# Kernel tuning notes

Measured on AMD Instinct MI355X. Metric: run time of the kernel, lower is better.

Reference implementation:

```python
import jax, jax.numpy as jnp
import numpy as np

D = 1024          # dim_in == dim_out
H = 16            # num_heads
G = 4             # num_kv_groups
HD = D // H       # head_dim = 64
GS = H // G       # group_size = 4
S = 2048          # context_length / seq_len
B = 2
EPS = 1e-05


def setup_inputs() -> dict:
    key = jax.random.key(0)
    ks = jax.random.split(key, 12)
    sd = 0.02
    return {
        "x":  jax.random.normal(ks[0], (B, S, D), jnp.float32),
        # torch.nn.Linear weights are stored [out_features, in_features]
        "wq": jax.random.normal(ks[1], (D, D), jnp.float32) * sd,
        "wk": jax.random.normal(ks[2], (G * HD, D), jnp.float32) * sd,
        "wv": jax.random.normal(ks[3], (G * HD, D), jnp.float32) * sd,
        "wo": jax.random.normal(ks[4], (D, D), jnp.float32) * sd,
        "w1": jax.random.normal(ks[5], (4 * D, D), jnp.float32) * sd,
        "w2": jax.random.normal(ks[6], (D, 4 * D), jnp.float32) * sd,
        "g1": jnp.ones((D,), jnp.float32),
        "b1": jnp.zeros((D,), jnp.float32),
        "g2": jnp.ones((D,), jnp.float32),
        "b2": jnp.zeros((D,), jnp.float32),
    }


def _layernorm(x, gamma, beta):
    mean = jnp.mean(x, axis=-1, keepdims=True)
    var = jnp.var(x, axis=-1, keepdims=True)  # unbiased=False
    return (x - mean) * jax.lax.rsqrt(var + EPS) * gamma + beta


def _gelu_tanh(x):
    c = jnp.sqrt(jnp.asarray(2.0 / jnp.pi, x.dtype))
    return 0.5 * x * (1.0 + jnp.tanh(c * (x + 0.044715 * x ** 3)))


def _gqa(x, wq, wk, wv, wo):
    b, s, _ = x.shape
    q = (x @ wq.T).reshape(b, s, H, HD).transpose(0, 2, 1, 3)   # [B,H,S,hd]
    k = (x @ wk.T).reshape(b, s, G, HD).transpose(0, 2, 1, 3)   # [B,G,S,hd]
    v = (x @ wv.T).reshape(b, s, G, HD).transpose(0, 2, 1, 3)
    k = jnp.repeat(k, GS, axis=1)                               # [B,H,S,hd]
    v = jnp.repeat(v, GS, axis=1)
    scores = jnp.einsum('bhqd,bhkd->bhqk', q, k)                # [B,H,S,S]
    causal = jnp.tril(jnp.ones((s, s), bool))
    scores = jnp.where(causal, scores, -jnp.inf)
    attn = jax.nn.softmax(scores / jnp.sqrt(jnp.asarray(HD, scores.dtype)), axis=-1)
    ctx = jnp.einsum('bhqk,bhkd->bhqd', attn, v)                # [B,H,S,hd]
    ctx = ctx.transpose(0, 2, 1, 3).reshape(b, s, D)
    return ctx @ wo.T


def reference(x, wq, wk, wv, wo, w1, w2, g1, b1, g2, b2):
    h = x + _gqa(_layernorm(x, g1, b1), wq, wk, wv, wo)
    ff = _layernorm(h, g2, b2) @ w1.T
    ff = _gelu_tanh(ff) @ w2.T
    return h + ff
```

## Files before the change

kernel.cpp:

```cpp
#include <hip/hip_runtime.h>
#include <stdint.h>

typedef __bf16 bf16_t;
typedef bf16_t bf16x8 __attribute__((ext_vector_type(8)));
typedef bf16_t bf16x4 __attribute__((ext_vector_type(4)));
typedef float f32x4 __attribute__((ext_vector_type(4)));

#define DEVFN static __device__ __forceinline__

DEVFN void gload_lds16(const void* g, void* l) {
  __builtin_amdgcn_global_load_lds((const __attribute__((address_space(1))) void*)g,
                                   (__attribute__((address_space(3))) void*)l, 16, 0, 0);
}

DEVFN float gelu_f(float x) {
  float u = 0.7978845608028654f * (x + 0.044715f * x * x * x);
  float e = __expf(2.0f * u);
  float t = 1.0f - 2.0f / (e + 1.0f);
  return 0.5f * x * (1.0f + t);
}

template <int CTRL>
DEVFN float dpp_rot(float x) {
  int i = __builtin_bit_cast(int, x);
  int r = __builtin_amdgcn_update_dpp(i, i, CTRL, 0xF, 0xF, false);
  return __builtin_bit_cast(float, r);
}
DEVFN float dpp_sum16(float x) {
  x += dpp_rot<0x121>(x);
  x += dpp_rot<0x122>(x);
  x += dpp_rot<0x124>(x);
  x += dpp_rot<0x128>(x);
  return x;
}

DEVFN void ln_row_body(const float* __restrict__ in, const float* __restrict__ gamma,
                       const float* __restrict__ beta, bf16_t* __restrict__ out,
                       int row, int tid, float* ss, float* qs) {
  const float4 v = ((const float4*)(in + (size_t)row * 1024))[tid];
  float s = v.x + v.y + v.z + v.w;
  float q = v.x * v.x + v.y * v.y + v.z * v.z + v.w * v.w;
#pragma unroll
  for (int off = 1; off < 64; off <<= 1) {
    s += __shfl_xor(s, off);
    q += __shfl_xor(q, off);
  }
  if ((tid & 63) == 0) { ss[tid >> 6] = s; qs[tid >> 6] = q; }
  __syncthreads();
  s = ss[0] + ss[1] + ss[2] + ss[3];
  q = qs[0] + qs[1] + qs[2] + qs[3];
  const float mean = s * (1.0f / 1024.0f);
  const float var = q * (1.0f / 1024.0f) - mean * mean;
  const float rstd = rsqrtf(var + 1e-5f);
  const float4 g4 = ((const float4*)gamma)[tid];
  const float4 b4 = ((const float4*)beta)[tid];
  bf16x4 o;
  o[0] = (bf16_t)((v.x - mean) * rstd * g4.x + b4.x);
  o[1] = (bf16_t)((v.y - mean) * rstd * g4.y + b4.y);
  o[2] = (bf16_t)((v.z - mean) * rstd * g4.z + b4.z);
  o[3] = (bf16_t)((v.w - mean) * rstd * g4.w + b4.w);
  *(bf16x4*)(out + (size_t)row * 1024 + tid * 4) = o;
}

DEVFN void cvt_quad(const float* __restrict__ s, bf16_t* __restrict__ d, int j) {
  float4 v = ((const float4*)s)[j];
  bf16x4 o;
  o[0] = (bf16_t)v.x; o[1] = (bf16_t)v.y; o[2] = (bf16_t)v.z; o[3] = (bf16_t)v.w;
  ((bf16x4*)d)[j] = o;
}

static __device__ const int kPrefix16[16] = {0,1,2,3,4,6,8,10,12,15,18,21,24,28,32,36};

DEVFN void combine_body(const bf16_t* __restrict__ pO, const float* __restrict__ pL,
                        bf16_t* __restrict__ ctx, int i, int h, int b, int tid) {
  const int C = (i >> 2) + 1;
  const int base = (b * 16 + h) * 40 + kPrefix16[i];
  const int row = tid >> 1;
  const int half = (tid & 1) * 32;
  float L = 0.0f, acc[32];
#pragma unroll
  for (int e = 0; e < 32; ++e) acc[e] = 0.0f;
  for (int c = 0; c < C; ++c) {
    L += pL[(size_t)(base + c) * 128 + row];
    const bf16_t* op = pO + ((size_t)(base + c) * 128 + row) * 64 + half;
#pragma unroll
    for (int j = 0; j < 4; ++j) {
      bf16x8 v = *(const bf16x8*)(op + j * 8);
#pragma unroll
      for (int e = 0; e < 8; ++e) acc[j * 8 + e] += (float)v[e];
    }
  }
  const float inv = 1.0f / L;
  bf16_t* outp = ctx + ((size_t)b * 2048 + i * 128 + row) * 1024 + h * 64 + half;
#pragma unroll
  for (int j = 0; j < 4; ++j) {
    bf16x8 o;
#pragma unroll
    for (int e = 0; e < 8; ++e) o[e] = (bf16_t)(acc[j * 8 + e] * inv);
    *(bf16x8*)(outp + j * 8) = o;
  }
}

__global__ __launch_bounds__(256) void prep1_kernel(const float* __restrict__ x,
                                                    const float* __restrict__ g1,
                                                    const float* __restrict__ b1,
                                                    bf16_t* __restrict__ h1,
                                                    const float* __restrict__ wq,
                                                    const float* __restrict__ wk,
                                                    const float* __restrict__ wv,
                                                    const float* __restrict__ wo,
                                                    bf16_t* __restrict__ qkv_dst,
                                                    bf16_t* __restrict__ wo_dst) {
  __shared__ float ss[4], qs[4];
  if (blockIdx.x < 4096) {
    ln_row_body(x, g1, b1, h1, blockIdx.x, threadIdx.x, ss, qs);
  } else {
    int i = (blockIdx.x - 4096) * 256 + threadIdx.x;
    const int stride = 2048 * 256;
    for (; i < 655360; i += stride) {
      if (i < 262144)      cvt_quad(wq, qkv_dst, i);
      else if (i < 327680) cvt_quad(wk, qkv_dst + 1048576, i - 262144);
      else if (i < 393216) cvt_quad(wv, qkv_dst + 1310720, i - 327680);
      else                 cvt_quad(wo, wo_dst, i - 393216);
    }
  }
}

__global__ __launch_bounds__(256) void prep2_kernel(const bf16_t* __restrict__ pO,
                                                    const float* __restrict__ pL,
                                                    bf16_t* __restrict__ ctx,
                                                    const float* __restrict__ w1,
                                                    bf16_t* __restrict__ w1_b) {
  if (blockIdx.x < 512) {
    const int i = blockIdx.x & 15;
    const int h = (blockIdx.x >> 4) & 15;
    const int b = blockIdx.x >> 8;
    combine_body(pO, pL, ctx, i, h, b, threadIdx.x);
  } else {
    const int i = (blockIdx.x - 512) * 256 + threadIdx.x;
    cvt_quad(w1, w1_b, i);
  }
}

__global__ __launch_bounds__(256) void prep3_kernel(const float* __restrict__ hres,
                                                    const float* __restrict__ g2,
                                                    const float* __restrict__ b2,
                                                    bf16_t* __restrict__ h2,
                                                    const float* __restrict__ w2,
                                                    bf16_t* __restrict__ w2_b) {
  __shared__ float ss[4], qs[4];
  if (blockIdx.x < 4096) {
    ln_row_body(hres, g2, b2, h2, blockIdx.x, threadIdx.x, ss, qs);
  } else {
    const int i = (blockIdx.x - 4096) * 256 + threadIdx.x;
    cvt_quad(w2, w2_b, i);
  }
}

template <int EPI, int BM>
__global__ __launch_bounds__(256, (BM == 64 ? 3 : 2))
void gemm_bt(const bf16_t* __restrict__ A, const bf16_t* __restrict__ W,
             bf16_t* outb, float* outf, const float* resid, int M, int N, int K) {
  constexpr int MI = BM / 32;
  constexpr int WRS = BM / 2;
  __shared__ __align__(16) bf16_t As[2][2][BM * 32];
  __shared__ __align__(16) bf16_t Bs[2][2][128 * 32];
  const int tid = threadIdx.x;
  const int lane = tid & 63;
  const int wid = tid >> 6;
  const int l15 = lane & 15;
  const int l4 = lane >> 4;

  const int nwg = gridDim.x * gridDim.y;
  const int bid = blockIdx.y * gridDim.x + blockIdx.x;
  const int cpx = nwg >> 3;
  const int swz = (bid & 7) * cpx + (bid >> 3);
  const int m0 = (swz / gridDim.x) * BM;
  const int n0 = (swz % gridDim.x) * 128;

  const int wr = wid >> 1;
  const int wc = wid & 1;

  const int sr = lane >> 2;
  const int sk = (lane & 3) * 8;
  const bf16_t* aBase;
  if constexpr (BM == 128) aBase = A + (size_t)(m0 + wid * 32 + sr) * K + sk;
  else                     aBase = A + (size_t)(m0 + wid * 16 + sr) * K + sk;
  const bf16_t* bBase = W + (size_t)(n0 + wid * 32 + sr) * K + sk;
  const size_t rowOff16 = (size_t)16 * K;

  f32x4 acc[MI][4] = {};
  const int NT = K / 64;

  auto stage = [&](int buf, int t) {
    const int kt = t * 64;
#pragma unroll
    for (int kk = 0; kk < 2; ++kk) {
      const int ko = kt + kk * 32;
      if constexpr (BM == 128) {
        gload_lds16(aBase + ko, &As[buf][kk][wid * 1024]);
        gload_lds16(aBase + ko + rowOff16, &As[buf][kk][wid * 1024 + 512]);
      } else {
        gload_lds16(aBase + ko, &As[buf][kk][wid * 512]);
      }
      gload_lds16(bBase + ko, &Bs[buf][kk][wid * 1024]);
      gload_lds16(bBase + ko + rowOff16, &Bs[buf][kk][wid * 1024 + 512]);
    }
  };

  stage(0, 0);
  for (int t = 0; t < NT; ++t) {
    __syncthreads();
    if (t + 1 < NT) stage((t + 1) & 1, t + 1);
    const int buf = t & 1;
#pragma unroll
    for (int kk = 0; kk < 2; ++kk) {
      bf16x8 af[MI], bfr[4];
#pragma unroll
      for (int i = 0; i < MI; ++i)
        af[i] = *(const bf16x8*)&As[buf][kk][(wr * WRS + i * 16 + l15) * 32 + l4 * 8];
#pragma unroll
      for (int j = 0; j < 4; ++j)
        bfr[j] = *(const bf16x8*)&Bs[buf][kk][(wc * 64 + j * 16 + l15) * 32 + l4 * 8];
#pragma unroll
      for (int i = 0; i < MI; ++i)
#pragma unroll
        for (int j = 0; j < 4; ++j)
          acc[i][j] = __builtin_amdgcn_mfma_f32_16x16x32_bf16(af[i], bfr[j], acc[i][j], 0, 0, 0);
    }
  }

  const int col0 = n0 + wc * 64 + l15;
  const int row0 = m0 + wr * WRS + l4 * 4;
#pragma unroll
  for (int i = 0; i < MI; ++i) {
#pragma unroll
    for (int r = 0; r < 4; ++r) {
      const size_t row = (size_t)(row0 + i * 16 + r);
#pragma unroll
      for (int j = 0; j < 4; ++j) {
        const size_t idx = row * N + col0 + j * 16;
        const float v = acc[i][j][r];
        if constexpr (EPI == 0) {
          outb[idx] = (bf16_t)v;
        } else if constexpr (EPI == 1) {
          outb[idx] = (bf16_t)gelu_f(v);
        } else {
          outf[idx] = resid[idx] + v;
        }
      }
    }
  }
}

static __device__ const int kQbTab[40] = {0,1,2,3,4,4,5,5,6,6,7,7,8,8,8,9,9,9,10,10,10,
                                          11,11,11,12,12,12,12,13,13,13,13,14,14,14,14,15,15,15,15};
static __device__ const int kCTab[40]  = {0,0,0,0,0,1,0,1,0,1,0,1,0,1,2,0,1,2,0,1,2,
                                          0,1,2,0,1,2,3,0,1,2,3,0,1,2,3,0,1,2,3};

__global__ __launch_bounds__(256, 3) void attn_kernel(const bf16_t* __restrict__ qkv,
                                                      bf16_t* __restrict__ pO,
                                                      float* __restrict__ pL) {
  __shared__ __align__(16) bf16_t Ks[2][64 * 68];
  __shared__ __align__(16) bf16_t Vt[2][64 * 68];
  __shared__ __align__(16) bf16_t Ps[4][32 * 68];
  const int tid = threadIdx.x, lane = tid & 63, wid = tid >> 6;
  const int l15 = lane & 15, l4 = lane >> 4;
  const int bx = blockIdx.x;
  const int qb = kQbTab[bx] * 128;
  const int kv_lo = kCTab[bx] * 512;
  const int kv_hi = min(qb + 128, kv_lo + 512);
  const int h = blockIdx.y, b = blockIdx.z;
  const int g = h >> 2;
  const int slot = (b * 16 + h) * 40 + bx;
  const size_t RS = 1536;
  const bf16_t* qbase = qkv + (size_t)b * 2048 * RS + h * 64;
  const bf16_t* kbase = qkv + (size_t)b * 2048 * RS + 1024 + g * 64;
  const bf16_t* vbase = kbase + 256;
  const float CE = 0.125f;

  bf16x8 qf[2][2];
#pragma unroll
  for (int rf = 0; rf < 2; ++rf)
#pragma unroll
    for (int kc = 0; kc < 2; ++kc) {
      bf16x8 raw = *(const bf16x8*)(qbase + (size_t)(qb + wid * 32 + rf * 16 + l15) * RS +
                                    kc * 32 + l4 * 8);
#pragma unroll
      for (int e = 0; e < 8; ++e) qf[rf][kc][e] = (bf16_t)((float)raw[e] * CE);
    }

  f32x4 po[2][4] = {};
  float l_i[2][4] = {};

  const int sKrow = tid >> 2, sKc = (tid & 3) * 16;
  const int sVkey = tid & 63, sVd = (tid >> 6) * 16;
  const bf16_t* kRowPtr = kbase + (size_t)sKrow * RS + sKc;
  const bf16_t* vRowPtr = vbase + (size_t)sVkey * RS + sVd;

  uint4 k0 = *(const uint4*)(kRowPtr + (size_t)kv_lo * RS);
  uint4 k1 = *(const uint4*)(kRowPtr + (size_t)kv_lo * RS + 8);
  bf16x8 v0 = *(const bf16x8*)(vRowPtr + (size_t)kv_lo * RS);
  bf16x8 v1 = *(const bf16x8*)(vRowPtr + (size_t)kv_lo * RS + 8);
  *(uint4*)&Ks[0][sKrow * 68 + sKc] = k0;
  *(uint4*)&Ks[0][sKrow * 68 + sKc + 8] = k1;
#pragma unroll
  for (int i = 0; i < 8; ++i) {
    Vt[0][(sVd + i) * 68 + sVkey] = v0[i];
    Vt[0][(sVd + 8 + i) * 68 + sVkey] = v1[i];
  }

  const int fb0 = qb + wid * 32;
  int cur = 0;
  for (int kv0 = kv_lo; kv0 < kv_hi; kv0 += 64) {
    __syncthreads();
    const bool more = (kv0 + 64) < kv_hi;
    if (more) {
      const bf16_t* kp = kRowPtr + (size_t)(kv0 + 64) * RS;
      const bf16_t* vp = vRowPtr + (size_t)(kv0 + 64) * RS;
      k0 = *(const uint4*)kp;
      k1 = *(const uint4*)(kp + 8);
      v0 = *(const bf16x8*)vp;
      v1 = *(const bf16x8*)(vp + 8);
    }

    f32x4 sAcc[2][4] = {};
#pragma unroll
    for (int jt = 0; jt < 4; ++jt) {
#pragma unroll
      for (int kc = 0; kc < 2; ++kc) {
        bf16x8 kf = *(const bf16x8*)&Ks[cur][(jt * 16 + l15) * 68 + kc * 32 + l4 * 8];
        sAcc[0][jt] = __builtin_amdgcn_mfma_f32_16x16x32_bf16(qf[0][kc], kf, sAcc[0][jt], 0, 0, 0);
        sAcc[1][jt] = __builtin_amdgcn_mfma_f32_16x16x32_bf16(qf[1][kc], kf, sAcc[1][jt], 0, 0, 0);
      }
    }

#pragma unroll
    for (int rf = 0; rf < 2; ++rf) {
      const int fb = fb0 + rf * 16;
      if (kv0 > fb + 15) continue;
      bf16_t* psb = &Ps[wid][(rf * 16 + l4 * 4) * 68 + l15];
      float rsum[4] = {0.f, 0.f, 0.f, 0.f};
      const bool diag = (kv0 + 63 > fb);
#pragma unroll
      for (int jt = 0; jt < 4; ++jt)
#pragma unroll
        for (int r = 0; r < 4; ++r) {
          float sv = sAcc[rf][jt][r];
          if (diag) {
            const int key = kv0 + jt * 16 + l15;
            sv = (key <= fb + l4 * 4 + r) ? sv : -3.0e38f;
          }
          const float e = __expf(sv);
          rsum[r] += e;
          psb[r * 68 + jt * 16] = (bf16_t)e;
        }
#pragma unroll
      for (int r = 0; r < 4; ++r) l_i[rf][r] += dpp_sum16(rsum[r]);
    }

    if (kv0 <= fb0 + 31) {
      const bool do0 = (kv0 <= fb0 + 15);
#pragma unroll
      for (int kc = 0; kc < 2; ++kc) {
        bf16x8 pa1 = *(const bf16x8*)&Ps[wid][(16 + l15) * 68 + kc * 32 + l4 * 8];
        bf16x8 pa0;
        if (do0) pa0 = *(const bf16x8*)&Ps[wid][l15 * 68 + kc * 32 + l4 * 8];
#pragma unroll
        for (int jd = 0; jd < 4; ++jd) {
          bf16x8 vf = *(const bf16x8*)&Vt[cur][(jd * 16 + l15) * 68 + kc * 32 + l4 * 8];
          if (do0) po[0][jd] = __builtin_amdgcn_mfma_f32_16x16x32_bf16(pa0, vf, po[0][jd], 0, 0, 0);
          po[1][jd] = __builtin_amdgcn_mfma_f32_16x16x32_bf16(pa1, vf, po[1][jd], 0, 0, 0);
        }
      }
    }

    if (more) {
      *(uint4*)&Ks[cur ^ 1][sKrow * 68 + sKc] = k0;
      *(uint4*)&Ks[cur ^ 1][sKrow * 68 + sKc + 8] = k1;
#pragma unroll
      for (int i = 0; i < 8; ++i) {
        Vt[cur ^ 1][(sVd + i) * 68 + sVkey] = v0[i];
        Vt[cur ^ 1][(sVd + 8 + i) * 68 + sVkey] = v1[i];
      }
    }
    cur ^= 1;
  }

#pragma unroll
  for (int rf = 0; rf < 2; ++rf) {
#pragma unroll
    for (int r = 0; r < 4; ++r) {
      const int lrow = wid * 32 + rf * 16 + l4 * 4 + r;
      if (l15 == 0) pL[(size_t)slot * 128 + lrow] = l_i[rf][r];
#pragma unroll
      for (int jd = 0; jd < 4; ++jd)
        pO[((size_t)slot * 128 + lrow) * 64 + jd * 16 + l15] = (bf16_t)po[rf][jd][r];
    }
  }
}

extern "C" void kernel_launch(void* const* d_in, const int* in_sizes, int n_in,
                              void* d_out, int out_size, void* d_ws, size_t ws_size,
                              hipStream_t stream) {
  const float* x = (const float*)d_in[0];
  const float* wq = (const float*)d_in[1];
  const float* wk = (const float*)d_in[2];
  const float* wv = (const float*)d_in[3];
  const float* wo = (const float*)d_in[4];
  const float* w1 = (const float*)d_in[5];
  const float* w2 = (const float*)d_in[6];
  const float* g1 = (const float*)d_in[7];
  const float* b1 = (const float*)d_in[8];
  const float* g2 = (const float*)d_in[9];
  const float* b2 = (const float*)d_in[10];
  float* out = (float*)d_out;

  char* ws = (char*)d_ws;
  bf16_t* qkv = (bf16_t*)(ws + 0);
  bf16_t* ctx = (bf16_t*)(ws + 12582912);
  bf16_t* wo_b = (bf16_t*)(ws + 20971520);
  bf16_t* wqkv_b = (bf16_t*)(ws + 23068672);
  bf16_t* h1 = (bf16_t*)(ws + 26214400);
  bf16_t* pO = (bf16_t*)(ws + 23068672);
  float* pL = (float*)(ws + 45088768);
  bf16_t* w1_b = (bf16_t*)(ws + 0);
  bf16_t* w2_b = (bf16_t*)(ws + 8388608);
  bf16_t* h2 = (bf16_t*)(ws + 16777216);
  bf16_t* ff = (bf16_t*)(ws + 25165824);

  prep1_kernel<<<6144, 256, 0, stream>>>(x, g1, b1, h1, wq, wk, wv, wo, wqkv_b, wo_b);
  gemm_bt<0, 64><<<dim3(12, 64), 256, 0, stream>>>(h1, wqkv_b, qkv, nullptr, nullptr, 4096, 1536, 1024);
  attn_kernel<<<dim3(40, 16, 2), 256, 0, stream>>>(qkv, pO, pL);
  prep2_kernel<<<4608, 256, 0, stream>>>(pO, pL, ctx, w1, w1_b);
  gemm_bt<2, 64><<<dim3(8, 64), 256, 0, stream>>>(ctx, wo_b, nullptr, out, x, 4096, 1024, 1024);
  prep3_kernel<<<8192, 256, 0, stream>>>(out, g2, b2, h2, w2, w2_b);
  gemm_bt<1, 128><<<dim3(32, 32), 256, 0, stream>>>(h2, w1_b, ff, nullptr, nullptr, 4096, 4096, 1024);
  gemm_bt<2, 64><<<dim3(8, 64), 256, 0, stream>>>(ff, w2_b, nullptr, out, out, 4096, 1024, 4096);
}
```

Before: 238.2 us.

## Split-K the final FFN down-projection GEMM with bf16 partial and add kernel

The last GEMM (K=4096) is split into two K halves over a z grid dimension and switched to 128-row tiles. Half 0 writes the residual sum to out, half 1 writes a bf16 partial to the workspace, and a new elementwise kernel adds the partial into out. This gives the down-projection more parallel work per CU and shorter K loops. The cost is an extra launch, extra memory traffic, and bf16 rounding of half the partial sum.

```diff
diff --git a/kernel.cpp b/kernel.cpp
--- a/kernel.cpp
+++ b/kernel.cpp
@@ -157,10 +157,22 @@
   }
 }
 
+__global__ __launch_bounds__(256) void ff2add_kernel(float* __restrict__ out,
+                                                     const bf16_t* __restrict__ p1) {
+  const int i = blockIdx.x * 256 + threadIdx.x;
+  bf16x8 v = ((const bf16x8*)p1)[i];
+  float4 a = ((const float4*)out)[2 * i];
+  float4 b = ((const float4*)out)[2 * i + 1];
+  a.x += (float)v[0]; a.y += (float)v[1]; a.z += (float)v[2]; a.w += (float)v[3];
+  b.x += (float)v[4]; b.y += (float)v[5]; b.z += (float)v[6]; b.w += (float)v[7];
+  ((float4*)out)[2 * i] = a;
+  ((float4*)out)[2 * i + 1] = b;
+}
+
 template <int EPI, int BM>
 __global__ __launch_bounds__(256, (BM == 64 ? 3 : 2))
 void gemm_bt(const bf16_t* __restrict__ A, const bf16_t* __restrict__ W,
-             bf16_t* outb, float* outf, const float* resid, int M, int N, int K) {
+             bf16_t* outb, float* outf, const float* resid, int M, int N, int K, int KL) {
   constexpr int MI = BM / 32;
   constexpr int WRS = BM / 2;
   __shared__ __align__(16) bf16_t As[2][2][BM * 32];
@@ -177,6 +189,7 @@
   const int swz = (bid & 7) * cpx + (bid >> 3);
   const int m0 = (swz / gridDim.x) * BM;
   const int n0 = (swz % gridDim.x) * 128;
+  const int kOff = blockIdx.z * KL;
 
   const int wr = wid >> 1;
   const int wc = wid & 1;
@@ -184,13 +197,13 @@
   const int sr = lane >> 2;
   const int sk = (lane & 3) * 8;
   const bf16_t* aBase;
-  if constexpr (BM == 128) aBase = A + (size_t)(m0 + wid * 32 + sr) * K + sk;
-  else                     aBase = A + (size_t)(m0 + wid * 16 + sr) * K + sk;
-  const bf16_t* bBase = W + (size_t)(n0 + wid * 32 + sr) * K + sk;
+  if constexpr (BM == 128) aBase = A + (size_t)(m0 + wid * 32 + sr) * K + sk + kOff;
+  else                     aBase = A + (size_t)(m0 + wid * 16 + sr) * K + sk + kOff;
+  const bf16_t* bBase = W + (size_t)(n0 + wid * 32 + sr) * K + sk + kOff;
   const size_t rowOff16 = (size_t)16 * K;
 
   f32x4 acc[MI][4] = {};
-  const int NT = K / 64;
+  const int NT = KL / 64;
 
   auto stage = [&](int buf, int t) {
     const int kt = t * 64;
@@ -245,8 +258,11 @@
           outb[idx] = (bf16_t)v;
         } else if constexpr (EPI == 1) {
           outb[idx] = (bf16_t)gelu_f(v);
+        } else if constexpr (EPI == 2) {
+          outf[idx] = resid[idx] + v;
         } else {
-          outf[idx] = resid[idx] + v;
+          if (blockIdx.z == 0) outf[idx] = resid[idx] + v;
+          else                 outb[idx] = (bf16_t)v;
         }
       }
     }
@@ -428,13 +444,19 @@
   bf16_t* w2_b = (bf16_t*)(ws + 8388608);
   bf16_t* h2 = (bf16_t*)(ws + 16777216);
   bf16_t* ff = (bf16_t*)(ws + 25165824);
+  bf16_t* p1 = (bf16_t*)(ws + 16777216);
 
   prep1_kernel<<<6144, 256, 0, stream>>>(x, g1, b1, h1, wq, wk, wv, wo, wqkv_b, wo_b);
-  gemm_bt<0, 64><<<dim3(12, 64), 256, 0, stream>>>(h1, wqkv_b, qkv, nullptr, nullptr, 4096, 1536, 1024);
+  gemm_bt<0, 64><<<dim3(12, 64), 256, 0, stream>>>(h1, wqkv_b, qkv, nullptr, nullptr,
+                                                   4096, 1536, 1024, 1024);
   attn_kernel<<<dim3(40, 16, 2), 256, 0, stream>>>(qkv, pO, pL);
   prep2_kernel<<<4608, 256, 0, stream>>>(pO, pL, ctx, w1, w1_b);
-  gemm_bt<2, 64><<<dim3(8, 64), 256, 0, stream>>>(ctx, wo_b, nullptr, out, x, 4096, 1024, 1024);
+  gemm_bt<2, 64><<<dim3(8, 64), 256, 0, stream>>>(ctx, wo_b, nullptr, out, x,
+                                                  4096, 1024, 1024, 1024);
   prep3_kernel<<<8192, 256, 0, stream>>>(out, g2, b2, h2, w2, w2_b);
-  gemm_bt<1, 128><<<dim3(32, 32), 256, 0, stream>>>(h2, w1_b, ff, nullptr, nullptr, 4096, 4096, 1024);
-  gemm_bt<2, 64><<<dim3(8, 64), 256, 0, stream>>>(ff, w2_b, nullptr, out, out, 4096, 1024, 4096);
-}
+  gemm_bt<1, 128><<<dim3(32, 32), 256, 0, stream>>>(h2, w1_b, ff, nullptr, nullptr,
+                                                    4096, 4096, 1024, 1024);
+  gemm_bt<3, 128><<<dim3(8, 32, 2), 256, 0, stream>>>(ff, w2_b, p1, out, out,
+                                                      4096, 1024, 4096, 2048);
+  ff2add_kernel<<<2048, 256, 0, stream>>>(out, p1);
+}
```

Measured after the change: 240.8 us. Within noise of the previous version (+1.1%).
